# Kernel optimization log

Hardware: AMD Instinct MI355X
Metric: run time of the kernel (lower is better)

The kernel has to match this reference:

```python
import jax, jax.numpy as jnp
import numpy as np
from jax import lax

N = 100000
E = 1600000
IN_C = 128
HID = 128
OUT_C = 64
NUM_CLASSES = 40
BN_EPS = 1e-5


def gcn_conv(x, row, col, W, b):
    # x: [N, F_in] -> [N, F_out]; PyG GCNConv: self-loops + sym normalization
    h = x @ W                                   # [N, F_out]
    loops = jnp.arange(N, dtype=row.dtype)
    r = jnp.concatenate([row, loops])           # [E+N]
    c = jnp.concatenate([col, loops])
    ones = jnp.ones(r.shape[0], dtype=x.dtype)
    deg = jax.ops.segment_sum(ones, c, num_segments=N)
    dinv = jnp.where(deg > 0, lax.rsqrt(deg), jnp.zeros_like(deg))
    norm = dinv[r] * dinv[c]                    # [E+N]
    msg = h[r] * norm[:, None]                  # gather + scale  [E+N, F_out]
    out = jax.ops.segment_sum(msg, c, num_segments=N)
    return out + b


def setup_inputs() -> dict:
    key = jax.random.key(0)
    ks = jax.random.split(key, 16)
    def glorot(k, shape):
        lim = float(np.sqrt(6.0 / (shape[0] + shape[1])))
        return jax.random.uniform(k, shape, jnp.float32, -lim, lim)
    x = jax.random.normal(ks[0], (N, IN_C), jnp.float32)
    edge_index = jax.random.randint(ks[1], (2, E), 0, N, jnp.int64)
    return {
        "x": x,
        "edge_index": edge_index,
        "w1": glorot(ks[2], (IN_C, HID)), "b1": jnp.zeros((HID,), jnp.float32),
        "w2": glorot(ks[3], (HID, HID)), "b2": jnp.zeros((HID,), jnp.float32),
        "bn_gamma": jnp.ones((HID,), jnp.float32), "bn_beta": jnp.zeros((HID,), jnp.float32),
        "bn_mean": jnp.zeros((HID,), jnp.float32), "bn_var": jnp.ones((HID,), jnp.float32),
        "cls_w": glorot(ks[4], (HID, OUT_C)), "cls_b": jnp.zeros((OUT_C,), jnp.float32),
        "sim_w": glorot(ks[5], (HID, NUM_CLASSES)), "sim_b": jnp.zeros((NUM_CLASSES,), jnp.float32),
        "hom_w": glorot(ks[6], (HID, 1)), "hom_b": jnp.zeros((1,), jnp.float32),
        "ent_w": glorot(ks[7], (HID, 1)), "ent_b": jnp.zeros((1,), jnp.float32),
    }


def reference(x, edge_index, w1, b1, w2, b2, bn_gamma, bn_beta, bn_mean, bn_var,
              cls_w, cls_b, sim_w, sim_b, hom_w, hom_b, ent_w, ent_b):
    row, col = edge_index[0], edge_index[1]
    # layer 1: GCNConv -> BN (eval) -> ReLU (dropout is identity in eval)
    h = gcn_conv(x, row, col, w1, b1)
    h = (h - bn_mean) * lax.rsqrt(bn_var + BN_EPS) * bn_gamma + bn_beta
    h = jax.nn.relu(h)
    # layer 2
    h = gcn_conv(h, row, col, w2, b2)
    main_out = jax.nn.log_softmax(h @ cls_w + cls_b, axis=1)
    sim_out = jax.nn.softmax(h @ sim_w + sim_b, axis=1)
    hom_out = jax.nn.sigmoid((h @ hom_w + hom_b)[:, 0])
    ent_out = jax.nn.sigmoid((h @ ent_w + ent_b)[:, 0])
    return (main_out, sim_out, hom_out, ent_out)
```

## Files before the change

### kernel.cpp

```cpp
#include <hip/hip_runtime.h>
#include <hip/hip_bf16.h>
#include <math.h>

#define N_NODES 100000
#define N_EDGES 1600000
#define F 128
#define OUT_C 64
#define NUM_CLASSES 40
#define BN_EPS 1e-5f

#define NBUCK 782
#define BCAP 4096
#define FILL_BLOCKS 512
#define EPB ((N_EDGES + FILL_BLOCKS - 1) / FILL_BLOCKS)

#define TSTRIDE 136

typedef __hip_bfloat16 bf16;
typedef __attribute__((ext_vector_type(8))) short bf16x8;
typedef __attribute__((ext_vector_type(4))) float f32x4;

#define PW1 0
#define PB1 16384
#define PW2 16512
#define PB2 32896
#define PGAMMA 33024
#define PBETA 33152
#define PMEAN 33280
#define PVAR 33408
#define PCLSW 33536
#define PCLSB 41728
#define PSIMW 41792
#define PSIMB 46912
#define PHOMW 46952
#define PHOMB 47080
#define PENTW 47081
#define PENTB 47209
#define PRAW_TOTAL 47210
#define PFW 47232
#define PFB 63616
#define PTOTAL 63744

__device__ __forceinline__ float uasf(unsigned u) { return __uint_as_float(u); }
__device__ __forceinline__ unsigned f2bu(float f) {
    bf16 h = __float2bfloat16(f);
    return (unsigned)*(unsigned short*)&h;
}

__global__ void detect_kernel(const void* __restrict__ x, const void* __restrict__ ei,
                              int* __restrict__ flags) {
    if (blockIdx.x != 0 || threadIdx.x != 0) return;
    const unsigned* xw = (const unsigned*)x;
    int votes = 0;
    for (int i = 0; i < 64; i++) {
        unsigned w = xw[i];
        unsigned e = (w >> 23) & 0xFFu;
        if (w == 0u || (e >= 90u && e <= 160u)) votes++;
    }
    flags[0] = (votes >= 48) ? 1 : 0;
    const unsigned* ew = (const unsigned*)ei;
    int zero_odd = 0;
    for (int i = 0; i < 64; i++)
        if (ew[2 * i + 1] == 0u) zero_odd++;
    flags[1] = (zero_odd >= 60) ? 1 : 0;
}

struct ParamSegs {
    const void* src[16];
    int dst[16];
};

__global__ void cvtparams_kernel(ParamSegs segs, float* __restrict__ params,
                                 const int* __restrict__ flags) {
    int idx = blockIdx.x * 256 + threadIdx.x;
    if (idx >= PRAW_TOTAL) return;
    int k = 0;
#pragma unroll
    for (int s = 1; s < 16; s++)
        if (idx >= segs.dst[s]) k = s;
    int rel = idx - segs.dst[k];
    const void* sp = segs.src[k];
    float v = flags[0] ? ((const float*)sp)[rel]
                       : __bfloat162float(((const bf16*)sp)[rel]);
    params[idx] = v;
}

__device__ __forceinline__ int load_edge(const int* __restrict__ ei, int which, int i, int i64) {
    size_t elem = (size_t)which * N_EDGES + (size_t)i;
    return i64 ? ei[elem * 2] : ei[elem];
}

__global__ __launch_bounds__(256) void fill2_kernel(const int* __restrict__ ei,
                                                    int* __restrict__ bcur,
                                                    int* __restrict__ srcBuck,
                                                    const int* __restrict__ flags) {
    __shared__ int hist[NBUCK];
    __shared__ int gbase[NBUCK];
    __shared__ int lcur[NBUCK];
    int blk = blockIdx.x;
    int t = threadIdx.x;
    int i64 = flags[1];
    int e0 = blk * EPB;
    int ecnt = N_EDGES - e0;
    if (ecnt > EPB) ecnt = EPB;
    for (int i = t; i < NBUCK; i += 256) hist[i] = 0;
    __syncthreads();
    for (int i = t; i < ecnt; i += 256) {
        int c = load_edge(ei, 1, e0 + i, i64);
        atomicAdd(&hist[c >> 7], 1);
    }
    __syncthreads();
    for (int i = t; i < NBUCK; i += 256) {
        int c = hist[i];
        gbase[i] = (c > 0) ? atomicAdd(&bcur[i], c) : 0;
        lcur[i] = 0;
    }
    __syncthreads();
    for (int i = t; i < ecnt; i += 256) {
        int c = load_edge(ei, 1, e0 + i, i64);
        int r = load_edge(ei, 0, e0 + i, i64);
        int b = c >> 7;
        int p = gbase[b] + atomicAdd(&lcur[b], 1);
        if (p < BCAP) srcBuck[b * BCAP + p] = ((c & 127) << 17) | r;
    }
}

__global__ __launch_bounds__(256) void bucketcnt_kernel(const int* __restrict__ srcBuck,
                                                        const int* __restrict__ bcur,
                                                        float* __restrict__ dinv) {
    __shared__ int dcnt[128];
    int b = blockIdx.x;
    int t = threadIdx.x;
    if (t < 128) dcnt[t] = 0;
    __syncthreads();
    int cnt = bcur[b];
    if (cnt > BCAP) cnt = BCAP;
    for (int i = t; i < cnt; i += 256) atomicAdd(&dcnt[srcBuck[b * BCAP + i] >> 17], 1);
    __syncthreads();
    if (t < 128) {
        int n = (b << 7) + t;
        if (n < N_NODES) dinv[n] = rsqrtf((float)(dcnt[t] + 1));
    }
}

__global__ void cvtx_kernel(const void* __restrict__ x, const float* __restrict__ dinv,
                            unsigned short* __restrict__ B16, const int* __restrict__ flags) {
    int i4 = blockIdx.x * blockDim.x + threadIdx.x;
    if (i4 >= N_NODES * F / 4) return;
    int n = i4 >> 5;
    float d = dinv[n];
    float v0, v1, v2, v3;
    if (flags[0]) {
        float4 v = ((const float4*)x)[i4];
        v0 = v.x; v1 = v.y; v2 = v.z; v3 = v.w;
    } else {
        uint2 u = ((const uint2*)x)[i4];
        v0 = uasf(u.x << 16);
        v1 = uasf(u.x & 0xFFFF0000u);
        v2 = uasf(u.y << 16);
        v3 = uasf(u.y & 0xFFFF0000u);
    }
    uint2 o;
    o.x = f2bu(v0 * d) | (f2bu(v1 * d) << 16);
    o.y = f2bu(v2 * d) | (f2bu(v3 * d) << 16);
    ((uint2*)B16)[i4] = o;
}

__device__ __forceinline__ float headw(const float* __restrict__ p, int j, int c) {
    if (c < OUT_C) return p[PCLSW + j * OUT_C + c];
    if (c < OUT_C + NUM_CLASSES) return p[PSIMW + j * NUM_CLASSES + (c - OUT_C)];
    if (c == 104) return p[PHOMW + j];
    if (c == 105) return p[PENTW + j];
    return 0.f;
}

__global__ void fusew_kernel(float* __restrict__ params) {
    int idx = blockIdx.x * 256 + threadIdx.x;
    int k = idx >> 7;
    int c = idx & 127;
    float s = 0.f;
    for (int j = 0; j < 128; j++) s += params[PW2 + k * 128 + j] * headw(params, j, c);
    params[PFW + k * 128 + c] = s;
    if (k == 0) {
        float b = 0.f;
        for (int j = 0; j < 128; j++) b += params[PB2 + j] * headw(params, j, c);
        if (c < OUT_C) b += params[PCLSB + c];
        else if (c < OUT_C + NUM_CLASSES) b += params[PSIMB + c - OUT_C];
        else if (c == 104) b += params[PHOMB];
        else if (c == 105) b += params[PENTB];
        params[PFB + c] = b;
    }
}

__global__ void wcvt_kernel(const float* __restrict__ params, unsigned short* __restrict__ wt) {
    int idx = blockIdx.x * 256 + threadIdx.x;
    if (idx >= 32768) return;
    int which = idx >> 14;
    int local = idx & 16383;
    int n = local >> 7;
    int k = local & 127;
    int ksrc = which ? ((k & 7) * 16 + (k >> 3)) : k;
    float v = params[(which ? PFW : PW1) + ksrc * 128 + n];
    wt[(which << 14) + n * 128 + k] = (unsigned short)f2bu(v);
}

#define ACC8(u)                                \
    do {                                       \
        a[0] += uasf((u).x << 16);             \
        a[1] += uasf((u).x & 0xFFFF0000u);     \
        a[2] += uasf((u).y << 16);             \
        a[3] += uasf((u).y & 0xFFFF0000u);     \
        a[4] += uasf((u).z << 16);             \
        a[5] += uasf((u).z & 0xFFFF0000u);     \
        a[6] += uasf((u).w << 16);             \
        a[7] += uasf((u).w & 0xFFFF0000u);     \
    } while (0)

__global__ __launch_bounds__(512, 4) void aggemm_kernel(
    const unsigned short* __restrict__ IN16, const unsigned short* __restrict__ Wt,
    unsigned short* __restrict__ outB, void* __restrict__ out,
    const float* __restrict__ params, const float* __restrict__ dinv,
    const int* __restrict__ srcBuck, const int* __restrict__ bcur,
    int mode, const int* __restrict__ flags) {
    __shared__ int sorted[BCAP];
    __shared__ int dcnt[128], doff[128], dcur[128];
    __shared__ float sC1[128], sC2[128];
    __shared__ __align__(16) char scratch[128 * TSTRIDE * 2];
    int* raw = (int*)scratch;
    unsigned short* tile = (unsigned short*)scratch;

    int b = blockIdx.x;
    int t = threadIdx.x;

    if (t < 128) {
        if (mode) {
            float s = rsqrtf(params[PVAR + t] + BN_EPS) * params[PGAMMA + t];
            sC1[t] = s;
            sC2[t] = params[PB1 + t] * s + (params[PBETA + t] - params[PMEAN + t] * s);
        } else {
            sC1[t] = params[PFB + t];
        }
        dcnt[t] = 0;
    }
    __syncthreads();

    int cnt = bcur[b];
    if (cnt > BCAP) cnt = BCAP;
    for (int i = t; i < cnt; i += 512) {
        int e = srcBuck[b * BCAP + i];
        raw[i] = e;
        atomicAdd(&dcnt[e >> 17], 1);
    }
    __syncthreads();
    if (t < 128) doff[t] = dcnt[t];
    __syncthreads();
    for (int d = 1; d < 128; d <<= 1) {
        int add = 0;
        if (t < 128 && t >= d) add = doff[t - d];
        __syncthreads();
        if (t < 128) doff[t] += add;
        __syncthreads();
    }
    if (t < 128) {
        doff[t] -= dcnt[t];
        dcur[t] = 0;
    }
    __syncthreads();
    for (int i = t; i < cnt; i += 512) {
        int e = raw[i];
        int d = e >> 17;
        int r = atomicAdd(&dcur[d], 1);
        sorted[doff[d] + r] = e & 0x1FFFF;
    }
    __syncthreads();

    int g16 = t >> 4;
    int hl8 = (t & 15) << 3;
    int base = b << 7;
    for (int d = g16; d < 128; d += 32) {
        int n = base + d;
        uint4 pk = make_uint4(0u, 0u, 0u, 0u);
        if (n < N_NODES) {
            float a[8] = {0.f, 0.f, 0.f, 0.f, 0.f, 0.f, 0.f, 0.f};
            {
                uint4 u = *(const uint4*)(IN16 + ((size_t)n << 7) + hl8);
                ACC8(u);
            }
            int o = doff[d], k = dcnt[d];
            int j = 0;
            for (; j + 4 <= k; j += 4) {
                int s0 = sorted[o + j];
                int s1 = sorted[o + j + 1];
                int s2 = sorted[o + j + 2];
                int s3 = sorted[o + j + 3];
                uint4 u0 = *(const uint4*)(IN16 + ((size_t)s0 << 7) + hl8);
                uint4 u1 = *(const uint4*)(IN16 + ((size_t)s1 << 7) + hl8);
                uint4 u2 = *(const uint4*)(IN16 + ((size_t)s2 << 7) + hl8);
                uint4 u3 = *(const uint4*)(IN16 + ((size_t)s3 << 7) + hl8);
                ACC8(u0);
                ACC8(u1);
                ACC8(u2);
                ACC8(u3);
            }
            for (; j < k; j++) {
                int s0 = sorted[o + j];
                uint4 u0 = *(const uint4*)(IN16 + ((size_t)s0 << 7) + hl8);
                ACC8(u0);
            }
            float dn = dinv[n];
            pk.x = f2bu(a[0] * dn) | (f2bu(a[1] * dn) << 16);
            pk.y = f2bu(a[2] * dn) | (f2bu(a[3] * dn) << 16);
            pk.z = f2bu(a[4] * dn) | (f2bu(a[5] * dn) << 16);
            pk.w = f2bu(a[6] * dn) | (f2bu(a[7] * dn) << 16);
        }
        *(uint4*)((char*)tile + (size_t)d * (TSTRIDE * 2) + (hl8 << 1)) = pk;
    }
    __syncthreads();

    int w = t >> 6, lane = t & 63, m16 = lane & 15, quad = lane >> 4;
    int rloc = w * 16 + m16;

    f32x4 acc[8];
#pragma unroll
    for (int ct = 0; ct < 8; ct++) acc[ct] = (f32x4){0.f, 0.f, 0.f, 0.f};

#pragma unroll
    for (int kk = 0; kk < 4; kk++) {
        bf16x8 af = *(const bf16x8*)((char*)tile + (size_t)rloc * (TSTRIDE * 2) + kk * 64 + quad * 16);
#pragma unroll
        for (int ct = 0; ct < 8; ct++) {
            bf16x8 bfr = *(const bf16x8*)(Wt + (size_t)((ct * 16 + m16) * 128) + kk * 32 + (quad << 3));
            acc[ct] = __builtin_amdgcn_mfma_f32_16x16x32_bf16(af, bfr, acc[ct], 0, 0, 0);
        }
    }

    int rowbase = base + w * 16;
    int r0 = rowbase + quad * 4;
    if (mode) {
        float sc[8], of[8];
#pragma unroll
        for (int ct = 0; ct < 8; ct++) {
            sc[ct] = sC1[ct * 16 + m16];
            of[ct] = sC2[ct * 16 + m16];
        }
#pragma unroll
        for (int reg = 0; reg < 4; reg++) {
            int gr = r0 + reg;
            if (gr >= N_NODES) continue;
            float dn = dinv[gr];
            unsigned pk[4];
#pragma unroll
            for (int i = 0; i < 4; i++) {
                float v0 = fmaxf(acc[2 * i][reg] * sc[2 * i] + of[2 * i], 0.f) * dn;
                float v1 = fmaxf(acc[2 * i + 1][reg] * sc[2 * i + 1] + of[2 * i + 1], 0.f) * dn;
                pk[i] = f2bu(v0) | (f2bu(v1) << 16);
            }
            *(uint4*)(outB + (size_t)gr * 128 + (m16 << 3)) = make_uint4(pk[0], pk[1], pk[2], pk[3]);
        }
    } else {
        int isf = flags[0];
        const size_t OFF_SIM = (size_t)N_NODES * OUT_C;
        const size_t OFF_HOM = OFF_SIM + (size_t)N_NODES * NUM_CLASSES;
        const size_t OFF_ENT = OFF_HOM + (size_t)N_NODES;
        float* outf = (float*)out;
        bf16* outb = (bf16*)out;
        float fb[8];
#pragma unroll
        for (int ct = 0; ct < 8; ct++) fb[ct] = sC1[ct * 16 + m16];
#define STORE_OUT(idx, v)                        \
    do {                                         \
        if (isf) outf[(idx)] = (v);              \
        else outb[(idx)] = __float2bfloat16(v);  \
    } while (0)
#pragma unroll
        for (int reg = 0; reg < 4; reg++) {
            int gr = r0 + reg;
            bool vrow = (gr < N_NODES);
            float v[8];
#pragma unroll
            for (int ct = 0; ct < 8; ct++) v[ct] = acc[ct][reg] + fb[ct];
            float m = fmaxf(fmaxf(v[0], v[1]), fmaxf(v[2], v[3]));
            m = fmaxf(m, __shfl_xor(m, 1));
            m = fmaxf(m, __shfl_xor(m, 2));
            m = fmaxf(m, __shfl_xor(m, 4));
            m = fmaxf(m, __shfl_xor(m, 8));
            float S = expf(v[0] - m) + expf(v[1] - m) + expf(v[2] - m) + expf(v[3] - m);
            S += __shfl_xor(S, 1);
            S += __shfl_xor(S, 2);
            S += __shfl_xor(S, 4);
            S += __shfl_xor(S, 8);
            float lS = m + logf(S);
            if (vrow) {
#pragma unroll
                for (int ct = 0; ct < 4; ct++)
                    STORE_OUT((size_t)gr * OUT_C + ct * 16 + m16, v[ct] - lS);
            }
            bool has6 = (m16 < 8);
            float s4 = v[4], s5 = v[5], s6 = has6 ? v[6] : -INFINITY;
            float m2 = fmaxf(fmaxf(s4, s5), s6);
            m2 = fmaxf(m2, __shfl_xor(m2, 1));
            m2 = fmaxf(m2, __shfl_xor(m2, 2));
            m2 = fmaxf(m2, __shfl_xor(m2, 4));
            m2 = fmaxf(m2, __shfl_xor(m2, 8));
            float e4 = expf(s4 - m2), e5 = expf(s5 - m2), e6 = has6 ? expf(s6 - m2) : 0.f;
            float S2 = e4 + e5 + e6;
            S2 += __shfl_xor(S2, 1);
            S2 += __shfl_xor(S2, 2);
            S2 += __shfl_xor(S2, 4);
            S2 += __shfl_xor(S2, 8);
            float rS2 = 1.f / S2;
            if (vrow) {
                STORE_OUT(OFF_SIM + (size_t)gr * NUM_CLASSES + m16, e4 * rS2);
                STORE_OUT(OFF_SIM + (size_t)gr * NUM_CLASSES + 16 + m16, e5 * rS2);
                if (has6) STORE_OUT(OFF_SIM + (size_t)gr * NUM_CLASSES + 32 + m16, e6 * rS2);
                if (m16 == 8) STORE_OUT(OFF_HOM + gr, 1.f / (1.f + expf(-v[6])));
                if (m16 == 9) STORE_OUT(OFF_ENT + gr, 1.f / (1.f + expf(-v[6])));
            }
        }
#undef STORE_OUT
    }
}

extern "C" void kernel_launch(void* const* d_in, const int* in_sizes, int n_in,
                              void* d_out, int out_size, void* d_ws, size_t ws_size,
                              hipStream_t stream) {
    const void* x = d_in[0];
    const int* ei = (const int*)d_in[1];

    char* ws = (char*)d_ws;
    size_t o = 0;
    auto alloc = [&](size_t bytes) {
        size_t r = o;
        o = (o + bytes + 255) & ~(size_t)255;
        return r;
    };
    char* RA = ws + alloc((size_t)51 * 1024 * 1024);
    char* RB = ws + alloc((size_t)26 * 1024 * 1024);
    float* params = (float*)(ws + alloc((size_t)PTOTAL * 4));
    unsigned short* wt = (unsigned short*)(ws + alloc(65536));
    float* dinv = (float*)(ws + alloc((size_t)N_NODES * 4));
    int* bcur = (int*)(ws + alloc((size_t)(NBUCK + 8) * 4));
    int* flags = (int*)(ws + alloc(256));

    int* srcBuck = (int*)RA;
    unsigned short* B16 = (unsigned short*)(RA + 13u * 1024 * 1024);
    unsigned short* G16 = (unsigned short*)RB;

    detect_kernel<<<1, 64, 0, stream>>>(x, ei, flags);
    hipMemsetAsync(bcur, 0, (size_t)(NBUCK + 8) * 4, stream);

    ParamSegs segs;
    const int srcIdx[16] = {2, 3, 4, 5, 6, 7, 8, 9, 10, 11, 12, 13, 14, 15, 16, 17};
    const int dsts[16] = {PW1, PB1, PW2, PB2, PGAMMA, PBETA, PMEAN, PVAR,
                          PCLSW, PCLSB, PSIMW, PSIMB, PHOMW, PHOMB, PENTW, PENTB};
    for (int k = 0; k < 16; k++) {
        segs.src[k] = d_in[srcIdx[k]];
        segs.dst[k] = dsts[k];
    }
    cvtparams_kernel<<<(PRAW_TOTAL + 255) / 256, 256, 0, stream>>>(segs, params, flags);
    fusew_kernel<<<64, 256, 0, stream>>>(params);
    wcvt_kernel<<<128, 256, 0, stream>>>(params, wt);

    fill2_kernel<<<FILL_BLOCKS, 256, 0, stream>>>(ei, bcur, srcBuck, flags);
    bucketcnt_kernel<<<NBUCK, 256, 0, stream>>>(srcBuck, bcur, dinv);
    cvtx_kernel<<<(N_NODES * F / 4 + 255) / 256, 256, 0, stream>>>(x, dinv, B16, flags);

    aggemm_kernel<<<NBUCK, 512, 0, stream>>>(B16, wt, G16, nullptr, params, dinv,
                                             srcBuck, bcur, 1, flags);
    aggemm_kernel<<<NBUCK, 512, 0, stream>>>(G16, wt + 16384, nullptr, d_out, params, dinv,
                                             srcBuck, bcur, 0, flags);
}
```

Baseline: 431.7 us.

## Fuse degree counting into bucket fill and parallelize input format detection

Removes the separate bucket-count kernel by accumulating in-degrees with global atomics inside the fill kernel, and computes dinv on the fly in the x-conversion kernel. The fill kernel caches destination indices in registers so it reads the column array only once. Detection now uses a wave ballot instead of a serial loop, and the softmax/sigmoid epilogue switches to fast __expf/__logf. The per-edge global atomics on deg add contention and traffic, and the fast math intrinsics slightly reduce accuracy.

```diff
diff --git a/kernel.cpp b/kernel.cpp
--- a/kernel.cpp
+++ b/kernel.cpp
@@ -13,6 +13,7 @@
 #define BCAP 4096
 #define FILL_BLOCKS 512
 #define EPB ((N_EDGES + FILL_BLOCKS - 1) / FILL_BLOCKS)
+#define FILL_ITERS 13
 
 #define TSTRIDE 136
 
@@ -49,20 +50,20 @@
 
 __global__ void detect_kernel(const void* __restrict__ x, const void* __restrict__ ei,
                               int* __restrict__ flags) {
-    if (blockIdx.x != 0 || threadIdx.x != 0) return;
+    if (blockIdx.x != 0) return;
+    int t = threadIdx.x & 63;
     const unsigned* xw = (const unsigned*)x;
-    int votes = 0;
-    for (int i = 0; i < 64; i++) {
-        unsigned w = xw[i];
-        unsigned e = (w >> 23) & 0xFFu;
-        if (w == 0u || (e >= 90u && e <= 160u)) votes++;
-    }
-    flags[0] = (votes >= 48) ? 1 : 0;
+    unsigned w = xw[t];
+    unsigned e = (w >> 23) & 0xFFu;
+    bool vote = (w == 0u || (e >= 90u && e <= 160u));
+    unsigned long long m1 = __ballot(vote);
     const unsigned* ew = (const unsigned*)ei;
-    int zero_odd = 0;
-    for (int i = 0; i < 64; i++)
-        if (ew[2 * i + 1] == 0u) zero_odd++;
-    flags[1] = (zero_odd >= 60) ? 1 : 0;
+    bool zo = (ew[2 * t + 1] == 0u);
+    unsigned long long m2 = __ballot(zo);
+    if (t == 0) {
+        flags[0] = (__popcll(m1) >= 48) ? 1 : 0;
+        flags[1] = (__popcll(m2) >= 60) ? 1 : 0;
+    }
 }
 
 struct ParamSegs {
@@ -93,6 +94,7 @@
 __global__ __launch_bounds__(256) void fill2_kernel(const int* __restrict__ ei,
                                                     int* __restrict__ bcur,
                                                     int* __restrict__ srcBuck,
+                                                    int* __restrict__ deg,
                                                     const int* __restrict__ flags) {
     __shared__ int hist[NBUCK];
     __shared__ int gbase[NBUCK];
@@ -105,9 +107,16 @@
     if (ecnt > EPB) ecnt = EPB;
     for (int i = t; i < NBUCK; i += 256) hist[i] = 0;
     __syncthreads();
-    for (int i = t; i < ecnt; i += 256) {
-        int c = load_edge(ei, 1, e0 + i, i64);
-        atomicAdd(&hist[c >> 7], 1);
+    int ccache[FILL_ITERS];
+#pragma unroll
+    for (int it = 0; it < FILL_ITERS; ++it) {
+        int i = t + it * 256;
+        int c = -1;
+        if (i < ecnt) {
+            c = load_edge(ei, 1, e0 + i, i64);
+            atomicAdd(&hist[c >> 7], 1);
+        }
+        ccache[it] = c;
     }
     __syncthreads();
     for (int i = t; i < NBUCK; i += 256) {
@@ -116,39 +125,28 @@
         lcur[i] = 0;
     }
     __syncthreads();
-    for (int i = t; i < ecnt; i += 256) {
-        int c = load_edge(ei, 1, e0 + i, i64);
-        int r = load_edge(ei, 0, e0 + i, i64);
-        int b = c >> 7;
-        int p = gbase[b] + atomicAdd(&lcur[b], 1);
-        if (p < BCAP) srcBuck[b * BCAP + p] = ((c & 127) << 17) | r;
-    }
-}
-
-__global__ __launch_bounds__(256) void bucketcnt_kernel(const int* __restrict__ srcBuck,
-                                                        const int* __restrict__ bcur,
-                                                        float* __restrict__ dinv) {
-    __shared__ int dcnt[128];
-    int b = blockIdx.x;
-    int t = threadIdx.x;
-    if (t < 128) dcnt[t] = 0;
-    __syncthreads();
-    int cnt = bcur[b];
-    if (cnt > BCAP) cnt = BCAP;
-    for (int i = t; i < cnt; i += 256) atomicAdd(&dcnt[srcBuck[b * BCAP + i] >> 17], 1);
-    __syncthreads();
-    if (t < 128) {
-        int n = (b << 7) + t;
-        if (n < N_NODES) dinv[n] = rsqrtf((float)(dcnt[t] + 1));
-    }
-}
-
-__global__ void cvtx_kernel(const void* __restrict__ x, const float* __restrict__ dinv,
-                            unsigned short* __restrict__ B16, const int* __restrict__ flags) {
+#pragma unroll
+    for (int it = 0; it < FILL_ITERS; ++it) {
+        int i = t + it * 256;
+        if (i < ecnt) {
+            int c = ccache[it];
+            int r = load_edge(ei, 0, e0 + i, i64);
+            int b = c >> 7;
+            int p = gbase[b] + atomicAdd(&lcur[b], 1);
+            if (p < BCAP) srcBuck[b * BCAP + p] = ((c & 127) << 17) | r;
+            atomicAdd(&deg[c], 1);
+        }
+    }
+}
+
+__global__ void cvtx_kernel(const void* __restrict__ x, const int* __restrict__ deg,
+                            float* __restrict__ dinv, unsigned short* __restrict__ B16,
+                            const int* __restrict__ flags) {
     int i4 = blockIdx.x * blockDim.x + threadIdx.x;
     if (i4 >= N_NODES * F / 4) return;
     int n = i4 >> 5;
-    float d = dinv[n];
+    float d = rsqrtf((float)(deg[n] + 1));
+    if ((i4 & 31) == 0) dinv[n] = d;
     float v0, v1, v2, v3;
     if (flags[0]) {
         float4 v = ((const float4*)x)[i4];
@@ -384,12 +382,12 @@
             m = fmaxf(m, __shfl_xor(m, 2));
             m = fmaxf(m, __shfl_xor(m, 4));
             m = fmaxf(m, __shfl_xor(m, 8));
-            float S = expf(v[0] - m) + expf(v[1] - m) + expf(v[2] - m) + expf(v[3] - m);
+            float S = __expf(v[0] - m) + __expf(v[1] - m) + __expf(v[2] - m) + __expf(v[3] - m);
             S += __shfl_xor(S, 1);
             S += __shfl_xor(S, 2);
             S += __shfl_xor(S, 4);
             S += __shfl_xor(S, 8);
-            float lS = m + logf(S);
+            float lS = m + __logf(S);
             if (vrow) {
 #pragma unroll
                 for (int ct = 0; ct < 4; ct++)
@@ -402,7 +400,7 @@
             m2 = fmaxf(m2, __shfl_xor(m2, 2));
             m2 = fmaxf(m2, __shfl_xor(m2, 4));
             m2 = fmaxf(m2, __shfl_xor(m2, 8));
-            float e4 = expf(s4 - m2), e5 = expf(s5 - m2), e6 = has6 ? expf(s6 - m2) : 0.f;
+            float e4 = __expf(s4 - m2), e5 = __expf(s5 - m2), e6 = has6 ? __expf(s6 - m2) : 0.f;
             float S2 = e4 + e5 + e6;
             S2 += __shfl_xor(S2, 1);
             S2 += __shfl_xor(S2, 2);
@@ -413,8 +411,8 @@
                 STORE_OUT(OFF_SIM + (size_t)gr * NUM_CLASSES + m16, e4 * rS2);
                 STORE_OUT(OFF_SIM + (size_t)gr * NUM_CLASSES + 16 + m16, e5 * rS2);
                 if (has6) STORE_OUT(OFF_SIM + (size_t)gr * NUM_CLASSES + 32 + m16, e6 * rS2);
-                if (m16 == 8) STORE_OUT(OFF_HOM + gr, 1.f / (1.f + expf(-v[6])));
-                if (m16 == 9) STORE_OUT(OFF_ENT + gr, 1.f / (1.f + expf(-v[6])));
+                if (m16 == 8) STORE_OUT(OFF_HOM + gr, 1.f / (1.f + __expf(-v[6])));
+                if (m16 == 9) STORE_OUT(OFF_ENT + gr, 1.f / (1.f + __expf(-v[6])));
             }
         }
 #undef STORE_OUT
@@ -440,6 +438,7 @@
     unsigned short* wt = (unsigned short*)(ws + alloc(65536));
     float* dinv = (float*)(ws + alloc((size_t)N_NODES * 4));
     int* bcur = (int*)(ws + alloc((size_t)(NBUCK + 8) * 4));
+    int* deg = (int*)(ws + alloc((size_t)N_NODES * 4));
     int* flags = (int*)(ws + alloc(256));
 
     int* srcBuck = (int*)RA;
@@ -447,7 +446,7 @@
     unsigned short* G16 = (unsigned short*)RB;
 
     detect_kernel<<<1, 64, 0, stream>>>(x, ei, flags);
-    hipMemsetAsync(bcur, 0, (size_t)(NBUCK + 8) * 4, stream);
+    hipMemsetAsync(bcur, 0, (size_t)((char*)(deg + N_NODES) - (char*)bcur), stream);
 
     ParamSegs segs;
     const int srcIdx[16] = {2, 3, 4, 5, 6, 7, 8, 9, 10, 11, 12, 13, 14, 15, 16, 17};
@@ -461,9 +460,8 @@
     fusew_kernel<<<64, 256, 0, stream>>>(params);
     wcvt_kernel<<<128, 256, 0, stream>>>(params, wt);
 
-    fill2_kernel<<<FILL_BLOCKS, 256, 0, stream>>>(ei, bcur, srcBuck, flags);
-    bucketcnt_kernel<<<NBUCK, 256, 0, stream>>>(srcBuck, bcur, dinv);
-    cvtx_kernel<<<(N_NODES * F / 4 + 255) / 256, 256, 0, stream>>>(x, dinv, B16, flags);
+    fill2_kernel<<<FILL_BLOCKS, 256, 0, stream>>>(ei, bcur, srcBuck, deg, flags);
+    cvtx_kernel<<<(N_NODES * F / 4 + 255) / 256, 256, 0, stream>>>(x, deg, dinv, B16, flags);
 
     aggemm_kernel<<<NBUCK, 512, 0, stream>>>(B16, wt, G16, nullptr, params, dinv,
                                              srcBuck, bcur, 1, flags);
```

New measurement: 469.9 us. 8.8% more time.
